# Performance work log

Hardware: AMD Instinct MI355X
Metric: run time of the kernel (lower is better)

## Reference

```python
import jax, jax.numpy as jnp
import numpy as np

KQ = 512
NEG = -1e9


def setup_inputs() -> dict:
    key = jax.random.key(0)
    k1, k2, k3, k4, k5 = jax.random.split(key, 5)
    B, NQ, NK, D, V, O = 16, 1024, 2048, 512, 512, 256
    return {
        "keys": jax.random.normal(k1, (B, NK, D), dtype=jnp.float32),
        "queries": jax.random.normal(k2, (B, NQ, D), dtype=jnp.float32),
        "values": jax.random.normal(k3, (B, NK, V), dtype=jnp.float32),
        "mask": jax.random.randint(k4, (B, NQ, NK), 0, 2, dtype=jnp.int32),
        "W_resize": jax.random.normal(k5, (O, V), dtype=jnp.float32) * (1.0 / np.sqrt(V)),
        "b_resize": jnp.zeros((O,), dtype=jnp.float32),
    }


def reference(keys, queries, values, mask, W_resize, b_resize):
    # score: scaled dot product  [B, NQ, NK]
    logits = jnp.einsum("bqd,bkd->bqk", queries, keys) / jnp.sqrt(jnp.float32(KQ))
    logits = jnp.where(mask == 0, jnp.float32(NEG), logits)
    attn = jax.nn.softmax(logits, axis=-1)
    # context: [B, NQ, V]
    context = jnp.einsum("bqk,bkv->bqv", attn, values)
    # resize to out_size
    context = jnp.einsum("bqv,ov->bqo", context, W_resize) + b_resize
    return context
```

## Files before the change

### kernel.cpp

```cpp
#include <hip/hip_runtime.h>

#define BB   16
#define NQ   1024
#define NK   2048
#define DD   512
#define VV   512
#define OO   256
#define SCALE 0.044194173824159216f

typedef __attribute__((ext_vector_type(4))) float f32x4;
typedef __attribute__((ext_vector_type(8))) short s16x8;

#define AS1(p) ((const __attribute__((address_space(1))) void*)(p))
#define AS3(p) ((__attribute__((address_space(3))) void*)(p))

__device__ __forceinline__ unsigned short f2bf(float f) {
  unsigned u = __float_as_uint(f);
  u += 0x7fffu + ((u >> 16) & 1u);
  return (unsigned short)(u >> 16);
}
__device__ __forceinline__ float bf2f(unsigned short b) {
  return __uint_as_float(((unsigned)b) << 16);
}

__device__ __forceinline__ void gemm_bt_core(
    const unsigned short* __restrict__ Abase,
    const unsigned short* __restrict__ Bbase,
    int K,
    unsigned short* As, unsigned short* Bs,
    f32x4 acc[4][4])
{
  const int t = threadIdx.x;
  const int w = t >> 6;
  const int l = t & 63;
  const int srow = l >> 2;
  const int scol = (l & 3) * 8;
  const int r0 = (w * 2 + 0) * 16 + srow;
  const int r1 = (w * 2 + 1) * 16 + srow;
  const int lds0 = (w * 2 + 0) * 512 + l * 8;
  const int lds1 = (w * 2 + 1) * 512 + l * 8;
  const int wm = (w >> 1) * 64;
  const int wn = (w & 1) * 64;
  const int lm = l & 15;
  const int lq = l >> 4;

  for (int kt = 0; kt < K; kt += 32) {
    __builtin_amdgcn_global_load_lds(AS1(Abase + (size_t)r0 * K + kt + scol), AS3(As + lds0), 16, 0, 0);
    __builtin_amdgcn_global_load_lds(AS1(Abase + (size_t)r1 * K + kt + scol), AS3(As + lds1), 16, 0, 0);
    __builtin_amdgcn_global_load_lds(AS1(Bbase + (size_t)r0 * K + kt + scol), AS3(Bs + lds0), 16, 0, 0);
    __builtin_amdgcn_global_load_lds(AS1(Bbase + (size_t)r1 * K + kt + scol), AS3(Bs + lds1), 16, 0, 0);
    __syncthreads();
    s16x8 af[4], bfr[4];
    #pragma unroll
    for (int i = 0; i < 4; ++i) {
      af[i]  = *(const s16x8*)(As + (wm + i * 16 + lm) * 32 + lq * 8);
      bfr[i] = *(const s16x8*)(Bs + (wn + i * 16 + lm) * 32 + lq * 8);
    }
    #pragma unroll
    for (int mi = 0; mi < 4; ++mi)
      #pragma unroll
      for (int ni = 0; ni < 4; ++ni)
        acc[mi][ni] = __builtin_amdgcn_mfma_f32_16x16x32_bf16(af[mi], bfr[ni], acc[mi][ni], 0, 0, 0);
    __syncthreads();
  }
}


#define CS_STRIDE 136

__global__ __launch_bounds__(256)
void qk_kernel(const unsigned short* __restrict__ Qb,
               const unsigned short* __restrict__ Kb,
               unsigned short* __restrict__ S)
{
  const int b  = blockIdx.z;
  const int tm = blockIdx.y;
  const int tn = blockIdx.x;
  __shared__ unsigned short smem[128 * CS_STRIDE];
  unsigned short* As = smem;
  unsigned short* Bs = smem + 4096;
  unsigned short* Cs = smem;
  f32x4 acc[4][4];
  #pragma unroll
  for (int i = 0; i < 4; ++i)
    #pragma unroll
    for (int j = 0; j < 4; ++j) acc[i][j] = (f32x4){0.f, 0.f, 0.f, 0.f};

  gemm_bt_core(Qb + ((size_t)b * NQ + tm * 128) * DD,
               Kb + ((size_t)b * NK + tn * 128) * DD, DD, As, Bs, acc);

  const int t = threadIdx.x, w = t >> 6, l = t & 63;
  const int wm = (w >> 1) * 64, wn = (w & 1) * 64;
  const int lm = l & 15, lq = l >> 4;
  #pragma unroll
  for (int mi = 0; mi < 4; ++mi)
    #pragma unroll
    for (int ni = 0; ni < 4; ++ni)
      #pragma unroll
      for (int r = 0; r < 4; ++r)
        Cs[(wm + mi * 16 + lq * 4 + r) * CS_STRIDE + wn + ni * 16 + lm] =
            f2bf(acc[mi][ni][r] * SCALE);
  __syncthreads();
  const int trow = t >> 4, tcol = (t & 15) * 8;
  #pragma unroll
  for (int it = 0; it < 8; ++it) {
    const int row = it * 16 + trow;
    s16x8 v = *(const s16x8*)(Cs + row * CS_STRIDE + tcol);
    *(s16x8*)(S + ((size_t)b * NQ + tm * 128 + row) * NK + tn * 128 + tcol) = v;
  }
}

__global__ __launch_bounds__(256)
void softmax_kernel(unsigned short* __restrict__ S, const int* __restrict__ mask)
{
  const size_t row = blockIdx.x;
  unsigned short* p = S + row * NK;
  const int* mrow = mask + row * NK;
  const int t = threadIdx.x, w = t >> 6, l = t & 63;
  __shared__ float sm[4];
  __shared__ float ss[4];

  const int4 m0 = ((const int4*)mrow)[t * 2];
  const int4 m1 = ((const int4*)mrow)[t * 2 + 1];
  s16x8 v = ((const s16x8*)p)[t];
  float x[8];
  #pragma unroll
  for (int j = 0; j < 8; ++j) x[j] = bf2f((unsigned short)v[j]);
  x[0] = m0.x ? x[0] : -1e9f;  x[1] = m0.y ? x[1] : -1e9f;
  x[2] = m0.z ? x[2] : -1e9f;  x[3] = m0.w ? x[3] : -1e9f;
  x[4] = m1.x ? x[4] : -1e9f;  x[5] = m1.y ? x[5] : -1e9f;
  x[6] = m1.z ? x[6] : -1e9f;  x[7] = m1.w ? x[7] : -1e9f;

  float mx = x[0];
  #pragma unroll
  for (int j = 1; j < 8; ++j) mx = fmaxf(mx, x[j]);
  #pragma unroll
  for (int off = 32; off > 0; off >>= 1) mx = fmaxf(mx, __shfl_down(mx, off, 64));
  if (l == 0) sm[w] = mx;
  __syncthreads();
  const float bm = fmaxf(fmaxf(sm[0], sm[1]), fmaxf(sm[2], sm[3]));

  float e[8], s = 0.f;
  #pragma unroll
  for (int j = 0; j < 8; ++j) { e[j] = __expf(x[j] - bm); s += e[j]; }
  #pragma unroll
  for (int off = 32; off > 0; off >>= 1) s += __shfl_down(s, off, 64);
  if (l == 0) ss[w] = s;
  __syncthreads();
  const float inv = 1.f / (ss[0] + ss[1] + ss[2] + ss[3]);

  s16x8 o;
  #pragma unroll
  for (int j = 0; j < 8; ++j) o[j] = (short)f2bf(e[j] * inv);
  ((s16x8*)p)[t] = o;
}

__global__ __launch_bounds__(256)
void pv_kernel(const unsigned short* __restrict__ P,
               const unsigned short* __restrict__ Vt,
               unsigned short* __restrict__ Ctx)
{
  const int b  = blockIdx.z;
  const int tm = blockIdx.y;
  const int tn = blockIdx.x;
  __shared__ unsigned short smem[128 * CS_STRIDE];
  unsigned short* As = smem;
  unsigned short* Bs = smem + 4096;
  unsigned short* Cs = smem;
  f32x4 acc[4][4];
  #pragma unroll
  for (int i = 0; i < 4; ++i)
    #pragma unroll
    for (int j = 0; j < 4; ++j) acc[i][j] = (f32x4){0.f, 0.f, 0.f, 0.f};

  gemm_bt_core(P  + ((size_t)b * NQ + tm * 128) * NK,
               Vt + ((size_t)b * VV + tn * 128) * NK, NK, As, Bs, acc);

  const int t = threadIdx.x, w = t >> 6, l = t & 63;
  const int wm = (w >> 1) * 64, wn = (w & 1) * 64;
  const int lm = l & 15, lq = l >> 4;
  #pragma unroll
  for (int mi = 0; mi < 4; ++mi)
    #pragma unroll
    for (int ni = 0; ni < 4; ++ni)
      #pragma unroll
      for (int r = 0; r < 4; ++r)
        Cs[(wm + mi * 16 + lq * 4 + r) * CS_STRIDE + wn + ni * 16 + lm] =
            f2bf(acc[mi][ni][r]);
  __syncthreads();
  const int trow = t >> 4, tcol = (t & 15) * 8;
  #pragma unroll
  for (int it = 0; it < 8; ++it) {
    const int row = it * 16 + trow;
    s16x8 v = *(const s16x8*)(Cs + row * CS_STRIDE + tcol);
    *(s16x8*)(Ctx + ((size_t)b * NQ + tm * 128 + row) * VV + tn * 128 + tcol) = v;
  }
}

#define CSF_STRIDE 136
__global__ __launch_bounds__(256)
void rs_kernel(const unsigned short* __restrict__ Ctx,
               const unsigned short* __restrict__ Wb,
               const float* __restrict__ bias,
               float* __restrict__ out)
{
  const int tm = blockIdx.y;
  const int tn = blockIdx.x;
  __shared__ float smemf[128 * CSF_STRIDE];
  unsigned short* As = (unsigned short*)smemf;
  unsigned short* Bs = (unsigned short*)smemf + 4096;
  float* Cs = smemf;
  f32x4 acc[4][4];
  #pragma unroll
  for (int i = 0; i < 4; ++i)
    #pragma unroll
    for (int j = 0; j < 4; ++j) acc[i][j] = (f32x4){0.f, 0.f, 0.f, 0.f};

  gemm_bt_core(Ctx + (size_t)tm * 128 * VV,
               Wb + (size_t)tn * 128 * VV, VV, As, Bs, acc);

  const int t = threadIdx.x, w = t >> 6, l = t & 63;
  const int wm = (w >> 1) * 64, wn = (w & 1) * 64;
  const int lm = l & 15, lq = l >> 4;
  #pragma unroll
  for (int mi = 0; mi < 4; ++mi)
    #pragma unroll
    for (int ni = 0; ni < 4; ++ni)
      #pragma unroll
      for (int r = 0; r < 4; ++r)
        Cs[(wm + mi * 16 + lq * 4 + r) * CSF_STRIDE + wn + ni * 16 + lm] = acc[mi][ni][r];
  __syncthreads();
  const int trow = t >> 4, tcol = (t & 15) * 8;
  #pragma unroll
  for (int it = 0; it < 8; ++it) {
    const int row = it * 16 + trow;
    f32x4 a = *(const f32x4*)(Cs + row * CSF_STRIDE + tcol);
    f32x4 c = *(const f32x4*)(Cs + row * CSF_STRIDE + tcol + 4);
    const int gn = tn * 128 + tcol;
    const f32x4 b0 = *(const f32x4*)(bias + gn);
    const f32x4 b1 = *(const f32x4*)(bias + gn + 4);
    a += b0; c += b1;
    float* o = out + (size_t)(tm * 128 + row) * OO + gn;
    *(f32x4*)o = a;
    *(f32x4*)(o + 4) = c;
  }
}

__global__ __launch_bounds__(256)
void cvt_kernel(const float* __restrict__ in, unsigned short* __restrict__ out, int n8)
{
  const int i = blockIdx.x * 256 + threadIdx.x;
  if (i >= n8) return;
  const float4* p = (const float4*)in + (size_t)i * 2;
  const float4 a = p[0], b = p[1];
  s16x8 o;
  o[0] = (short)f2bf(a.x); o[1] = (short)f2bf(a.y);
  o[2] = (short)f2bf(a.z); o[3] = (short)f2bf(a.w);
  o[4] = (short)f2bf(b.x); o[5] = (short)f2bf(b.y);
  o[6] = (short)f2bf(b.z); o[7] = (short)f2bf(b.w);
  ((s16x8*)out)[i] = o;
}

#define VT_STRIDE 68
__global__ __launch_bounds__(256)
void vt_kernel(const float* __restrict__ V, unsigned short* __restrict__ Vt)
{
  const int b  = blockIdx.z;
  const int k0 = blockIdx.y * 64;
  const int v0 = blockIdx.x * 64;
  __shared__ float tile[64 * VT_STRIDE];
  const int t = threadIdx.x;
  const int lr = t >> 4, lc4 = (t & 15) * 4;
  #pragma unroll
  for (int j = 0; j < 4; ++j) {
    const int row = lr + j * 16;
    const float4 x = *(const float4*)(V + ((size_t)b * NK + k0 + row) * VV + v0 + lc4);
    *(float4*)(tile + row * VT_STRIDE + lc4) = x;
  }
  __syncthreads();
  const int vr = t >> 3, kx = (t & 7) * 8;
  #pragma unroll
  for (int j = 0; j < 2; ++j) {
    const int v = vr + j * 32;
    s16x8 o;
    #pragma unroll
    for (int i = 0; i < 8; ++i) o[i] = (short)f2bf(tile[(kx + i) * VT_STRIDE + v]);
    *(s16x8*)(Vt + ((size_t)b * VV + v0 + v) * NK + k0 + kx) = o;
  }
}

extern "C" void kernel_launch(void* const* d_in, const int* in_sizes, int n_in,
                              void* d_out, int out_size, void* d_ws, size_t ws_size,
                              hipStream_t stream)
{
  const float* keys    = (const float*)d_in[0];
  const float* queries = (const float*)d_in[1];
  const float* values  = (const float*)d_in[2];
  const int*   mask    = (const int*)  d_in[3];
  const float* W       = (const float*)d_in[4];
  const float* bias    = (const float*)d_in[5];
  float* out = (float*)d_out;

  char* ws = (char*)d_ws;
  unsigned short* Qb = (unsigned short*)(ws);
  unsigned short* Kb = (unsigned short*)(ws + (16ull << 20));
  unsigned short* Vt = (unsigned short*)(ws + (48ull << 20));
  unsigned short* Wb = (unsigned short*)(ws + (80ull << 20));
  unsigned short* S  = (unsigned short*)(ws + (81ull << 20));
  unsigned short* Ctx = Qb;

  cvt_kernel<<<dim3(4096), 256, 0, stream>>>(queries, Qb, (BB * NQ * DD) / 8);
  cvt_kernel<<<dim3(8192), 256, 0, stream>>>(keys, Kb, (BB * NK * DD) / 8);
  cvt_kernel<<<dim3(64),   256, 0, stream>>>(W, Wb, (OO * VV) / 8);
  vt_kernel<<<dim3(VV / 64, NK / 64, BB), 256, 0, stream>>>(values, Vt);

  qk_kernel<<<dim3(NK / 128, NQ / 128, BB), 256, 0, stream>>>(Qb, Kb, S);
  softmax_kernel<<<dim3(BB * NQ), 256, 0, stream>>>(S, mask);
  pv_kernel<<<dim3(VV / 128, NQ / 128, BB), 256, 0, stream>>>(S, Vt, Ctx);
  rs_kernel<<<dim3(OO / 128, (BB * NQ) / 128, 1), 256, 0, stream>>>(Ctx, Wb, bias, out);
}
```

Baseline: 464.7 us.

## Fuse masked exp into QK epilogue and defer softmax normalization to PV

Removes the standalone softmax pass. The QK epilogue now applies the mask, exponentiates the scaled logits without max subtraction, writes unnormalized probabilities, and accumulates per-row sums with atomics. The PV epilogue divides by those row sums. This avoids a full read-modify-write of the score matrix. In exchange it drops max-subtraction, which risks overflow for large logits and a divide by zero for fully masked rows, and it adds atomics plus a zeroing kernel.

Result: no change. 460.9 us (-0.8%).

```diff
diff --git a/kernel.cpp b/kernel.cpp
--- a/kernel.cpp
+++ b/kernel.cpp
@@ -71,7 +71,9 @@
 __global__ __launch_bounds__(256)
 void qk_kernel(const unsigned short* __restrict__ Qb,
                const unsigned short* __restrict__ Kb,
-               unsigned short* __restrict__ S)
+               const int* __restrict__ mask,
+               unsigned short* __restrict__ S,
+               float* __restrict__ sums)
 {
   const int b  = blockIdx.z;
   const int tm = blockIdx.y;
@@ -101,72 +103,54 @@
         Cs[(wm + mi * 16 + lq * 4 + r) * CS_STRIDE + wn + ni * 16 + lm] =
             f2bf(acc[mi][ni][r] * SCALE);
   __syncthreads();
+
   const int trow = t >> 4, tcol = (t & 15) * 8;
   #pragma unroll
   for (int it = 0; it < 8; ++it) {
     const int row = it * 16 + trow;
+    const int gq = tm * 128 + row;
+    const size_t gbase = ((size_t)b * NQ + gq) * NK + tn * 128 + tcol;
     s16x8 v = *(const s16x8*)(Cs + row * CS_STRIDE + tcol);
-    *(s16x8*)(S + ((size_t)b * NQ + tm * 128 + row) * NK + tn * 128 + tcol) = v;
-  }
-}
-
-__global__ __launch_bounds__(256)
-void softmax_kernel(unsigned short* __restrict__ S, const int* __restrict__ mask)
-{
-  const size_t row = blockIdx.x;
-  unsigned short* p = S + row * NK;
-  const int* mrow = mask + row * NK;
-  const int t = threadIdx.x, w = t >> 6, l = t & 63;
-  __shared__ float sm[4];
-  __shared__ float ss[4];
-
-  const int4 m0 = ((const int4*)mrow)[t * 2];
-  const int4 m1 = ((const int4*)mrow)[t * 2 + 1];
-  s16x8 v = ((const s16x8*)p)[t];
-  float x[8];
-  #pragma unroll
-  for (int j = 0; j < 8; ++j) x[j] = bf2f((unsigned short)v[j]);
-  x[0] = m0.x ? x[0] : -1e9f;  x[1] = m0.y ? x[1] : -1e9f;
-  x[2] = m0.z ? x[2] : -1e9f;  x[3] = m0.w ? x[3] : -1e9f;
-  x[4] = m1.x ? x[4] : -1e9f;  x[5] = m1.y ? x[5] : -1e9f;
-  x[6] = m1.z ? x[6] : -1e9f;  x[7] = m1.w ? x[7] : -1e9f;
-
-  float mx = x[0];
-  #pragma unroll
-  for (int j = 1; j < 8; ++j) mx = fmaxf(mx, x[j]);
-  #pragma unroll
-  for (int off = 32; off > 0; off >>= 1) mx = fmaxf(mx, __shfl_down(mx, off, 64));
-  if (l == 0) sm[w] = mx;
-  __syncthreads();
-  const float bm = fmaxf(fmaxf(sm[0], sm[1]), fmaxf(sm[2], sm[3]));
-
-  float e[8], s = 0.f;
-  #pragma unroll
-  for (int j = 0; j < 8; ++j) { e[j] = __expf(x[j] - bm); s += e[j]; }
-  #pragma unroll
-  for (int off = 32; off > 0; off >>= 1) s += __shfl_down(s, off, 64);
-  if (l == 0) ss[w] = s;
-  __syncthreads();
-  const float inv = 1.f / (ss[0] + ss[1] + ss[2] + ss[3]);
-
-  s16x8 o;
-  #pragma unroll
-  for (int j = 0; j < 8; ++j) o[j] = (short)f2bf(e[j] * inv);
-  ((s16x8*)p)[t] = o;
+    const int4 m0 = *(const int4*)(mask + gbase);
+    const int4 m1 = *(const int4*)(mask + gbase + 4);
+    float e[8];
+    e[0] = m0.x ? __expf(bf2f((unsigned short)v[0])) : 0.f;
+    e[1] = m0.y ? __expf(bf2f((unsigned short)v[1])) : 0.f;
+    e[2] = m0.z ? __expf(bf2f((unsigned short)v[2])) : 0.f;
+    e[3] = m0.w ? __expf(bf2f((unsigned short)v[3])) : 0.f;
+    e[4] = m1.x ? __expf(bf2f((unsigned short)v[4])) : 0.f;
+    e[5] = m1.y ? __expf(bf2f((unsigned short)v[5])) : 0.f;
+    e[6] = m1.z ? __expf(bf2f((unsigned short)v[6])) : 0.f;
+    e[7] = m1.w ? __expf(bf2f((unsigned short)v[7])) : 0.f;
+    float sp = 0.f;
+    #pragma unroll
+    for (int j = 0; j < 8; ++j) sp += e[j];
+    #pragma unroll
+    for (int off = 8; off > 0; off >>= 1) sp += __shfl_down(sp, off, 16);
+    if ((t & 15) == 0) atomicAdd(&sums[(size_t)b * NQ + gq], sp);
+    s16x8 o;
+    #pragma unroll
+    for (int j = 0; j < 8; ++j) o[j] = (short)f2bf(e[j]);
+    *(s16x8*)(S + gbase) = o;
+  }
 }
 
 __global__ __launch_bounds__(256)
 void pv_kernel(const unsigned short* __restrict__ P,
                const unsigned short* __restrict__ Vt,
+               const float* __restrict__ sums,
                unsigned short* __restrict__ Ctx)
 {
   const int b  = blockIdx.z;
   const int tm = blockIdx.y;
   const int tn = blockIdx.x;
   __shared__ unsigned short smem[128 * CS_STRIDE];
+  __shared__ float Ls[128];
   unsigned short* As = smem;
   unsigned short* Bs = smem + 4096;
   unsigned short* Cs = smem;
+  const int t = threadIdx.x;
+  if (t < 128) Ls[t] = 1.0f / sums[(size_t)b * NQ + tm * 128 + t];
   f32x4 acc[4][4];
   #pragma unroll
   for (int i = 0; i < 4; ++i)
@@ -176,7 +160,7 @@
   gemm_bt_core(P  + ((size_t)b * NQ + tm * 128) * NK,
                Vt + ((size_t)b * VV + tn * 128) * NK, NK, As, Bs, acc);
 
-  const int t = threadIdx.x, w = t >> 6, l = t & 63;
+  const int w = t >> 6, l = t & 63;
   const int wm = (w >> 1) * 64, wn = (w & 1) * 64;
   const int lm = l & 15, lq = l >> 4;
   #pragma unroll
@@ -184,9 +168,10 @@
     #pragma unroll
     for (int ni = 0; ni < 4; ++ni)
       #pragma unroll
-      for (int r = 0; r < 4; ++r)
-        Cs[(wm + mi * 16 + lq * 4 + r) * CS_STRIDE + wn + ni * 16 + lm] =
-            f2bf(acc[mi][ni][r]);
+      for (int r = 0; r < 4; ++r) {
+        const int row = wm + mi * 16 + lq * 4 + r;
+        Cs[row * CS_STRIDE + wn + ni * 16 + lm] = f2bf(acc[mi][ni][r] * Ls[row]);
+      }
   __syncthreads();
   const int trow = t >> 4, tcol = (t & 15) * 8;
   #pragma unroll
@@ -289,6 +274,13 @@
   }
 }
 
+__global__ __launch_bounds__(256)
+void zero_kernel(float* __restrict__ p, int n)
+{
+  const int i = blockIdx.x * 256 + threadIdx.x;
+  if (i < n) p[i] = 0.f;
+}
+
 extern "C" void kernel_launch(void* const* d_in, const int* in_sizes, int n_in,
                               void* d_out, int out_size, void* d_ws, size_t ws_size,
                               hipStream_t stream)
@@ -307,15 +299,16 @@
   unsigned short* Vt = (unsigned short*)(ws + (48ull << 20));
   unsigned short* Wb = (unsigned short*)(ws + (80ull << 20));
   unsigned short* S  = (unsigned short*)(ws + (81ull << 20));
+  float* sums        = (float*)(ws + (145ull << 20));
   unsigned short* Ctx = Qb;
 
   cvt_kernel<<<dim3(4096), 256, 0, stream>>>(queries, Qb, (BB * NQ * DD) / 8);
   cvt_kernel<<<dim3(8192), 256, 0, stream>>>(keys, Kb, (BB * NK * DD) / 8);
   cvt_kernel<<<dim3(64),   256, 0, stream>>>(W, Wb, (OO * VV) / 8);
   vt_kernel<<<dim3(VV / 64, NK / 64, BB), 256, 0, stream>>>(values, Vt);
-
-  qk_kernel<<<dim3(NK / 128, NQ / 128, BB), 256, 0, stream>>>(Qb, Kb, S);
-  softmax_kernel<<<dim3(BB * NQ), 256, 0, stream>>>(S, mask);
-  pv_kernel<<<dim3(VV / 128, NQ / 128, BB), 256, 0, stream>>>(S, Vt, Ctx);
+  zero_kernel<<<dim3(64), 256, 0, stream>>>(sums, BB * NQ);
+
+  qk_kernel<<<dim3(NK / 128, NQ / 128, BB), 256, 0, stream>>>(Qb, Kb, mask, S, sums);
+  pv_kernel<<<dim3(VV / 128, NQ / 128, BB), 256, 0, stream>>>(S, Vt, sums, Ctx);
   rs_kernel<<<dim3(OO / 128, (BB * NQ) / 128, 1), 256, 0, stream>>>(Ctx, Wb, bias, out);
 }
```
